# Optimization experiments

Hardware: AMD Instinct MI355X
Metric: run time of the kernel (lower is better)

Reference implementation:

```python
import jax, jax.numpy as jnp
import numpy as np

EMBED_DIM = 1024
NUM_HEADS = 16
HEAD_DIM = EMBED_DIM // NUM_HEADS
STD = 0.02


def setup_inputs() -> dict:
    key = jax.random.key(0)
    k1, k2, k3 = jax.random.split(key, 3)
    B, S = 2, 2048
    inputs = jax.random.normal(k1, (B, S, EMBED_DIM), dtype=jnp.float32)
    # qkv projection: Linear(E, 3E); torch Linear weight is [out, in]
    w_qkv = jax.random.normal(k2, (3 * EMBED_DIM, EMBED_DIM), dtype=jnp.float32) * STD
    b_qkv = jnp.zeros((3 * EMBED_DIM,), dtype=jnp.float32)
    w_out = jax.random.normal(k3, (EMBED_DIM, EMBED_DIM), dtype=jnp.float32) * STD
    b_out = jnp.zeros((EMBED_DIM,), dtype=jnp.float32)
    return {"inputs": inputs, "w_qkv": w_qkv, "b_qkv": b_qkv, "w_out": w_out, "b_out": b_out}


def reference(inputs, w_qkv, b_qkv, w_out, b_out):
    B, S, E = inputs.shape
    qkv = inputs @ w_qkv.T + b_qkv                      # [B,S,3E]
    q, k, v = jnp.split(qkv, 3, axis=2)                 # each [B,S,E]

    def split_heads(t):
        return t.reshape(B, S, NUM_HEADS, HEAD_DIM).transpose(0, 2, 1, 3)  # [B,H,S,D]

    q, k, v = split_heads(q), split_heads(k), split_heads(v)
    scores = jnp.einsum('bhqd,bhkd->bhqk', q, k) * (1.0 / np.sqrt(HEAD_DIM))
    causal = jnp.tril(jnp.ones((S, S), dtype=bool))     # [S,S]
    scores = jnp.where(causal[None, None, :, :], scores, -jnp.inf)
    probs = jax.nn.softmax(scores, axis=-1)             # dropout is identity in eval mode
    ctx = jnp.einsum('bhqk,bhkd->bhqd', probs, v)       # [B,H,S,D]
    ctx = ctx.transpose(0, 2, 1, 3).reshape(B, S, E)
    return ctx @ w_out.T + b_out
```

## Files before the change

### kernel.cpp

```cpp
#include <hip/hip_runtime.h>
#include <hip/hip_bf16.h>

#define BATCH 2
#define SEQ   2048
#define EMB   1024
#define NHEAD 16
#define HDIM  64
#define MTOT  (BATCH*SEQ)
#define KTOT  EMB

#define NX  (MTOT*EMB)
#define NW1 (3*EMB*EMB)
#define NW2 (EMB*EMB)
#define NCVT (NX+NW1+NW2)

typedef short bf8 __attribute__((ext_vector_type(8)));
typedef short s4v __attribute__((ext_vector_type(4)));
typedef float f4  __attribute__((ext_vector_type(4)));
typedef unsigned int uint;

__device__ __forceinline__ short f2b(float f) {
    __hip_bfloat16 h = __float2bfloat16(f);
    return __builtin_bit_cast(short, h);
}
__device__ __forceinline__ void gl_lds16(const short* g, short* l) {
    __builtin_amdgcn_global_load_lds(
        (const __attribute__((address_space(1))) uint*)g,
        (__attribute__((address_space(3))) uint*)l, 16, 0, 0);
}
#define SWZ_SRC(lane)      ((((lane) ^ ((lane)>>2) ^ ((lane)>>4)) & 3) * 8)
#define SWZ_RD(quad, l16)  ((((quad) ^ (l16) ^ ((l16)>>2)) & 3) * 8)

__global__ __launch_bounds__(256) void cvt_all(
    const float* __restrict__ X, const float* __restrict__ W1,
    const float* __restrict__ W2,
    short* __restrict__ xb, short* __restrict__ w1b, short* __restrict__ w2b)
{
    int i4 = (blockIdx.x * 256 + threadIdx.x) * 4;
    const float* src; short* dst; int off;
    if (i4 < NX)            { src = X;  dst = xb;  off = i4; }
    else if (i4 < NX + NW1) { src = W1; dst = w1b; off = i4 - NX; }
    else                    { src = W2; dst = w2b; off = i4 - NX - NW1; }
    float4 v = *(const float4*)&src[off];
    s4v o; o[0]=f2b(v.x); o[1]=f2b(v.y); o[2]=f2b(v.z); o[3]=f2b(v.w);
    *(s4v*)&dst[off] = o;
}

__global__ __launch_bounds__(256) void gemm_qkv(
    const short* __restrict__ Xb, const short* __restrict__ Wb,
    const float* __restrict__ bias,
    short* __restrict__ qb, short* __restrict__ kb, short* __restrict__ vtb)
{
    __shared__ __align__(16) short As[2*128*32];
    __shared__ __align__(16) short Bs[2*128*32];
    const int tid  = threadIdx.x;
    const int lane = tid & 63;
    const int w    = tid >> 6;
    const int l16  = lane & 15, quad = lane >> 4;
    const int wm   = (w >> 1) * 64, wn = (w & 1) * 64;
    const int srow = (lane >> 2);
    const int scol = SWZ_SRC(lane);
    f4 acc[4][4] = {};
    for (int k0 = 0; k0 < KTOT; k0 += 64) {
        #pragma unroll
        for (int t = 0; t < 4; t++) {
            const int rr = w*32 + (t & 1)*16;
            const int kc = t >> 1;
            int ra = blockIdx.x*128 + rr + srow;
            gl_lds16(&Xb[(size_t)ra*KTOT + k0 + kc*32 + scol], &As[kc*4096 + rr*32]);
            int rb = blockIdx.y*128 + rr + srow;
            gl_lds16(&Wb[(size_t)rb*KTOT + k0 + kc*32 + scol], &Bs[kc*4096 + rr*32]);
        }
        __syncthreads();
        #pragma unroll
        for (int kc = 0; kc < 2; kc++) {
            bf8 af[4], bf[4];
            #pragma unroll
            for (int t = 0; t < 4; t++) {
                af[t] = *(const bf8*)&As[kc*4096 + (wm + t*16 + l16)*32 + SWZ_RD(quad, l16)];
                bf[t] = *(const bf8*)&Bs[kc*4096 + (wn + t*16 + l16)*32 + SWZ_RD(quad, l16)];
            }
            #pragma unroll
            for (int mt = 0; mt < 4; mt++)
                #pragma unroll
                for (int nt = 0; nt < 4; nt++)
                    acc[mt][nt] = __builtin_amdgcn_mfma_f32_16x16x32_bf16(af[mt], bf[nt], acc[mt][nt], 0, 0, 0);
        }
        __syncthreads();
    }
    #pragma unroll
    for (int mt = 0; mt < 4; mt++)
    #pragma unroll
    for (int nt = 0; nt < 4; nt++) {
        int colg = blockIdx.y*128 + wn + nt*16 + l16;
        float bv = bias[colg];
        #pragma unroll
        for (int r = 0; r < 4; r++) {
            int rowg = blockIdx.x*128 + wm + mt*16 + quad*4 + r;
            short h = f2b(acc[mt][nt][r] + bv);
            int bb = rowg >> 11, s = rowg & 2047;
            if (colg < 1024) {
                int hh = colg >> 6, d = colg & 63;
                qb[(((bb*NHEAD + hh)*SEQ + s) << 6) + d] = h;
            } else if (colg < 2048) {
                int c2 = colg - 1024, hh = c2 >> 6, d = c2 & 63;
                kb[(((bb*NHEAD + hh)*SEQ + s) << 6) + d] = h;
            } else {
                int c3 = colg - 2048, hh = c3 >> 6, d = c3 & 63;
                int ssw = (s & ~63) | (((s & 15) << 2) | ((s >> 4) & 3));
                vtb[((bb*NHEAD + hh)*HDIM + d)*SEQ + ssw] = h;
            }
        }
    }
}

__global__ __launch_bounds__(256, 4) void attn(
    const short* __restrict__ qb, const short* __restrict__ kb,
    const short* __restrict__ vtb, short* __restrict__ ctx)
{
    __shared__ __align__(16) short Ks[2*4096];
    __shared__ __align__(16) short Vs[2*4096];
    __shared__ __align__(16) short pl[4][16*64];
    const int tid = threadIdx.x;
    const int w = tid >> 6, lane = tid & 63;
    const int l16 = lane & 15, quad = lane >> 4;
    const int f  = blockIdx.x;
    const int bh = ((f & 7) << 2) + ((f >> 3) & 3);
    const int tq = 31 - (f >> 5);
    const int q0w = tq*64 + w*16;
    const int base = bh * (SEQ*HDIM);
    short* myp = pl[w];
    const float SC = 0.125f * 1.44269504f;

    const int lq  = lane >> 2;
    const int lsw = SWZ_SRC(lane);

    const bool isk = (w < 2);
    short* tb = isk ? Ks : Vs;
    const int sstep = isk ? 64*HDIM : 64;
    const short* sp0; const short* sp1; const short* sp2; const short* sp3;
    int dof[4];
    {
        const int wb2 = (w & 1) * 4;
        #pragma unroll
        for (int tt = 0; tt < 4; tt++) {
            int t = wb2 + tt, cc = t & 1, g = (t >> 1) & 3;
            dof[tt] = (cc*64 + g*16)*32;
            const short* s = isk ? &kb[base + (g*16 + lq)*HDIM + cc*32 + lsw]
                                 : &vtb[base + (g*16 + lq)*SEQ + cc*32 + lsw];
            if (tt == 0) sp0 = s; else if (tt == 1) sp1 = s;
            else if (tt == 2) sp2 = s; else sp3 = s;
        }
    }

    bf8 qa[2];
    #pragma unroll
    for (int kc = 0; kc < 2; kc++)
        qa[kc] = *(const bf8*)&qb[base + (q0w + l16)*HDIM + kc*32 + quad*8];

    f4 o[4] = {};
    float lacc[4] = {};
    const int rdK = l16*32 + SWZ_RD(quad, l16);

    gl_lds16(sp0, tb + dof[0]); gl_lds16(sp1, tb + dof[1]);
    gl_lds16(sp2, tb + dof[2]); gl_lds16(sp3, tb + dof[3]);
    sp0 += sstep; sp1 += sstep; sp2 += sstep; sp3 += sstep;
    __syncthreads();

    int buf = 0;
    for (int st = 0; st <= tq; st++) {
        if (st < tq) {
            short* d = tb + (buf ^ 1)*4096;
            gl_lds16(sp0, d + dof[0]); gl_lds16(sp1, d + dof[1]);
            gl_lds16(sp2, d + dof[2]); gl_lds16(sp3, d + dof[3]);
            sp0 += sstep; sp1 += sstep; sp2 += sstep; sp3 += sstep;
        }
        const int kbase = buf*4096 + rdK;
        f4 s[4] = {};
        #pragma unroll
        for (int kf = 0; kf < 4; kf++)
            #pragma unroll
            for (int c = 0; c < 2; c++) {
                bf8 kfr = *(const bf8*)&Ks[kbase + (c*64 + kf*16)*32];
                s[kf] = __builtin_amdgcn_mfma_f32_16x16x32_bf16(qa[c], kfr, s[kf], 0, 0, 0);
            }
        if (st == tq) {
            const int j0 = st*64;
            #pragma unroll
            for (int r = 0; r < 4; r++) {
                const int row = quad*4 + r;
                const int qi  = q0w + row;
                float e[4];
                #pragma unroll
                for (int kf = 0; kf < 4; kf++) {
                    e[kf] = __builtin_amdgcn_exp2f(s[kf][r] * SC);
                    if (j0 + kf*16 + l16 > qi) e[kf] = 0.0f;
                    lacc[r] += e[kf];
                }
                uint u01 = __builtin_amdgcn_perm(__builtin_bit_cast(uint, e[1]),
                                                 __builtin_bit_cast(uint, e[0]), 0x07060302u);
                uint u23 = __builtin_amdgcn_perm(__builtin_bit_cast(uint, e[3]),
                                                 __builtin_bit_cast(uint, e[2]), 0x07060302u);
                uint2 pk = {u01, u23};
                int c8 = ((l16 >> 1) ^ (row & 7));
                *(uint2*)&myp[row*64 + c8*8 + (l16 & 1)*4] = pk;
            }
        } else {
            #pragma unroll
            for (int r = 0; r < 4; r++) {
                const int row = quad*4 + r;
                float e[4];
                #pragma unroll
                for (int kf = 0; kf < 4; kf++) {
                    e[kf] = __builtin_amdgcn_exp2f(s[kf][r] * SC);
                    lacc[r] += e[kf];
                }
                uint u01 = __builtin_amdgcn_perm(__builtin_bit_cast(uint, e[1]),
                                                 __builtin_bit_cast(uint, e[0]), 0x07060302u);
                uint u23 = __builtin_amdgcn_perm(__builtin_bit_cast(uint, e[3]),
                                                 __builtin_bit_cast(uint, e[2]), 0x07060302u);
                uint2 pk = {u01, u23};
                int c8 = ((l16 >> 1) ^ (row & 7));
                *(uint2*)&myp[row*64 + c8*8 + (l16 & 1)*4] = pk;
            }
        }
        asm volatile("" ::: "memory");
        bf8 pa[2];
        #pragma unroll
        for (int kc = 0; kc < 2; kc++)
            pa[kc] = *(const bf8*)&myp[l16*64 + (((kc*4 + quad) ^ (l16 & 7)))*8];
        #pragma unroll
        for (int dt = 0; dt < 4; dt++)
            #pragma unroll
            for (int c = 0; c < 2; c++) {
                bf8 vf = *(const bf8*)&Vs[kbase + (c*64 + dt*16)*32];
                o[dt] = __builtin_amdgcn_mfma_f32_16x16x32_bf16(pa[c], vf, o[dt], 0, 0, 0);
            }
        __syncthreads();
        buf ^= 1;
    }
    #pragma unroll
    for (int r = 0; r < 4; r++) {
        float v = lacc[r];
        v += __shfl_xor(v, 1);
        v += __shfl_xor(v, 2);
        v += __shfl_xor(v, 4);
        v += __shfl_xor(v, 8);
        lacc[r] = v;
    }
    const int b = bh >> 4, h = bh & 15;
    #pragma unroll
    for (int r = 0; r < 4; r++) {
        float inv = 1.0f / lacc[r];
        int qi = q0w + quad*4 + r;
        int rowoff = (b*SEQ + qi)*EMB + h*HDIM;
        #pragma unroll
        for (int dt = 0; dt < 4; dt++)
            ctx[rowoff + dt*16 + l16] = f2b(o[dt][r] * inv);
    }
}

__global__ __launch_bounds__(256) void gemm_out(
    const short* __restrict__ A, const short* __restrict__ Wb,
    const float* __restrict__ bias, float* __restrict__ out)
{
    __shared__ __align__(16) short As[2*64*32];
    __shared__ __align__(16) short Bs[2*64*32];
    const int f = blockIdx.x;
    const int xcd = f & 7, i = f >> 3;
    const int by = xcd*2 + (i & 1);
    const int bx = i >> 1;
    const int tid  = threadIdx.x;
    const int lane = tid & 63;
    const int w    = tid >> 6;
    const int l16  = lane & 15, quad = lane >> 4;
    const int wm   = (w >> 1) * 32, wn = (w & 1) * 32;
    const int srow = (lane >> 2);
    const int scol = SWZ_SRC(lane);
    f4 acc[2][2] = {};
    for (int k0 = 0; k0 < KTOT; k0 += 64) {
        #pragma unroll
        for (int kc = 0; kc < 2; kc++) {
            int ra = bx*64 + w*16 + srow;
            gl_lds16(&A[(size_t)ra*KTOT + k0 + kc*32 + scol],  &As[kc*2048 + (w*16)*32]);
            int rb = by*64 + w*16 + srow;
            gl_lds16(&Wb[(size_t)rb*KTOT + k0 + kc*32 + scol], &Bs[kc*2048 + (w*16)*32]);
        }
        __syncthreads();
        #pragma unroll
        for (int kc = 0; kc < 2; kc++) {
            bf8 af[2], bf[2];
            #pragma unroll
            for (int t = 0; t < 2; t++) {
                af[t] = *(const bf8*)&As[kc*2048 + (wm + t*16 + l16)*32 + SWZ_RD(quad, l16)];
                bf[t] = *(const bf8*)&Bs[kc*2048 + (wn + t*16 + l16)*32 + SWZ_RD(quad, l16)];
            }
            #pragma unroll
            for (int mt = 0; mt < 2; mt++)
                #pragma unroll
                for (int nt = 0; nt < 2; nt++)
                    acc[mt][nt] = __builtin_amdgcn_mfma_f32_16x16x32_bf16(af[mt], bf[nt], acc[mt][nt], 0, 0, 0);
        }
        __syncthreads();
    }
    #pragma unroll
    for (int mt = 0; mt < 2; mt++)
    #pragma unroll
    for (int nt = 0; nt < 2; nt++) {
        int colg = by*64 + wn + nt*16 + l16;
        float bv = bias[colg];
        #pragma unroll
        for (int r = 0; r < 4; r++) {
            int rowg = bx*64 + wm + mt*16 + quad*4 + r;
            out[(size_t)rowg*EMB + colg] = acc[mt][nt][r] + bv;
        }
    }
}

extern "C" void kernel_launch(void* const* d_in, const int* in_sizes, int n_in,
                              void* d_out, int out_size, void* d_ws, size_t ws_size,
                              hipStream_t stream) {
    const float* X    = (const float*)d_in[0];
    const float* Wqkv = (const float*)d_in[1];
    const float* Bqkv = (const float*)d_in[2];
    const float* Wout = (const float*)d_in[3];
    const float* Bout = (const float*)d_in[4];
    float* out = (float*)d_out;

    short* xb    = (short*)d_ws;
    short* w1b   = xb  + NX;
    short* w2b   = w1b + NW1;
    short* qb    = w2b + NW2;
    short* kb    = qb  + NX;
    short* vtb   = kb  + NX;
    short* ctx   = vtb + NX;

    cvt_all<<<NCVT/1024, 256, 0, stream>>>(X, Wqkv, Wout, xb, w1b, w2b);
    dim3 g1(MTOT/128, 3*EMB/128);
    gemm_qkv<<<g1, 256, 0, stream>>>(xb, w1b, Bqkv, qb, kb, vtb);
    attn<<<dim3(1024), 256, 0, stream>>>(qb, kb, vtb, ctx);
    gemm_out<<<dim3(1024), 256, 0, stream>>>(ctx, w2b, Bout, out);
}
```

Before: 178.4 us.

## Software-pipeline QKV GEMM with register prefetch of next K tile

Replaces the direct global-to-LDS loads in the QKV projection GEMM with a register-staged prefetch. The next K tile is loaded into registers while MFMAs run on the current LDS tile, then written to LDS after a barrier. The aim is to hide global memory latency behind compute. The cost is extra VGPRs for the staged data and an explicit LDS write path in place of the direct-to-LDS loads.

```diff
diff --git a/kernel.cpp b/kernel.cpp
--- a/kernel.cpp
+++ b/kernel.cpp
@@ -60,31 +60,53 @@
     const int wm   = (w >> 1) * 64, wn = (w & 1) * 64;
     const int srow = (lane >> 2);
     const int scol = SWZ_SRC(lane);
+    const int lchunk = (lane & 3) * 8;
+
+    const short* gA[4]; const short* gB[4]; int ldsOff[4];
+    #pragma unroll
+    for (int t = 0; t < 4; t++) {
+        const int rr = w*32 + (t & 1)*16;
+        const int kc = t >> 1;
+        gA[t] = &Xb[(size_t)(blockIdx.x*128 + rr + srow)*KTOT + kc*32 + scol];
+        gB[t] = &Wb[(size_t)(blockIdx.y*128 + rr + srow)*KTOT + kc*32 + scol];
+        ldsOff[t] = kc*4096 + (rr + srow)*32 + lchunk;
+    }
+
     f4 acc[4][4] = {};
+    bf8 av[4], bv[4];
+    #pragma unroll
+    for (int t = 0; t < 4; t++) { av[t] = *(const bf8*)gA[t]; bv[t] = *(const bf8*)gB[t]; }
+    #pragma unroll
+    for (int t = 0; t < 4; t++) { *(bf8*)&As[ldsOff[t]] = av[t]; *(bf8*)&Bs[ldsOff[t]] = bv[t]; }
+    __syncthreads();
+
     for (int k0 = 0; k0 < KTOT; k0 += 64) {
-        #pragma unroll
-        for (int t = 0; t < 4; t++) {
-            const int rr = w*32 + (t & 1)*16;
-            const int kc = t >> 1;
-            int ra = blockIdx.x*128 + rr + srow;
-            gl_lds16(&Xb[(size_t)ra*KTOT + k0 + kc*32 + scol], &As[kc*4096 + rr*32]);
-            int rb = blockIdx.y*128 + rr + srow;
-            gl_lds16(&Wb[(size_t)rb*KTOT + k0 + kc*32 + scol], &Bs[kc*4096 + rr*32]);
-        }
-        __syncthreads();
+        const bool more = (k0 + 64) < KTOT;
+        if (more) {
+            #pragma unroll
+            for (int t = 0; t < 4; t++) {
+                av[t] = *(const bf8*)(gA[t] + k0 + 64);
+                bv[t] = *(const bf8*)(gB[t] + k0 + 64);
+            }
+        }
         #pragma unroll
         for (int kc = 0; kc < 2; kc++) {
-            bf8 af[4], bf[4];
+            bf8 af[4], bf_[4];
             #pragma unroll
             for (int t = 0; t < 4; t++) {
-                af[t] = *(const bf8*)&As[kc*4096 + (wm + t*16 + l16)*32 + SWZ_RD(quad, l16)];
-                bf[t] = *(const bf8*)&Bs[kc*4096 + (wn + t*16 + l16)*32 + SWZ_RD(quad, l16)];
+                af[t]  = *(const bf8*)&As[kc*4096 + (wm + t*16 + l16)*32 + SWZ_RD(quad, l16)];
+                bf_[t] = *(const bf8*)&Bs[kc*4096 + (wn + t*16 + l16)*32 + SWZ_RD(quad, l16)];
             }
             #pragma unroll
             for (int mt = 0; mt < 4; mt++)
                 #pragma unroll
                 for (int nt = 0; nt < 4; nt++)
-                    acc[mt][nt] = __builtin_amdgcn_mfma_f32_16x16x32_bf16(af[mt], bf[nt], acc[mt][nt], 0, 0, 0);
+                    acc[mt][nt] = __builtin_amdgcn_mfma_f32_16x16x32_bf16(af[mt], bf_[nt], acc[mt][nt], 0, 0, 0);
+        }
+        __syncthreads();
+        if (more) {
+            #pragma unroll
+            for (int t = 0; t < 4; t++) { *(bf8*)&As[ldsOff[t]] = av[t]; *(bf8*)&Bs[ldsOff[t]] = bv[t]; }
         }
         __syncthreads();
     }
@@ -93,11 +115,11 @@
     #pragma unroll
     for (int nt = 0; nt < 4; nt++) {
         int colg = blockIdx.y*128 + wn + nt*16 + l16;
-        float bv = bias[colg];
+        float bv2 = bias[colg];
         #pragma unroll
         for (int r = 0; r < 4; r++) {
             int rowg = blockIdx.x*128 + wm + mt*16 + quad*4 + r;
-            short h = f2b(acc[mt][nt][r] + bv);
+            short h = f2b(acc[mt][nt][r] + bv2);
             int bb = rowg >> 11, s = rowg & 2047;
             if (colg < 1024) {
                 int hh = colg >> 6, d = colg & 63;
```

Result: slower. 182.0 us (+2.0%).
